# Performance work log

Measured on AMD Instinct MI355X. Metric: run time of the kernel, lower is better.

## Reference

```python
import jax, jax.numpy as jnp
import numpy as np

EPS = 1e-5

def binarize(w):
    # sign() binarization with straight-through estimator (identity grad)
    s = jnp.where(w >= 0, 1.0, -1.0).astype(w.dtype)
    return w + jax.lax.stop_gradient(s - w)

def batchnorm(x, gamma, beta):
    # BatchNorm1d in training mode: biased batch statistics over axis 0
    mean = jnp.mean(x, axis=0)
    var = jnp.mean(jnp.square(x - mean), axis=0)
    return (x - mean) * jax.lax.rsqrt(var + EPS) * gamma + beta

def setup_inputs() -> dict:
    key = jax.random.key(0)
    ks = jax.random.split(key, 3)
    B, D_IN, D_H, D_OUT = 65536, 784, 300, 10
    x = jax.random.normal(ks[0], (B, D_IN), dtype=jnp.float32)
    W1 = jax.random.normal(ks[1], (D_H, D_IN), dtype=jnp.float32) * 0.05
    W2 = jax.random.normal(ks[2], (D_OUT, D_H), dtype=jnp.float32) * 0.05
    gamma1 = jnp.ones((D_H,), jnp.float32)
    beta1 = jnp.zeros((D_H,), jnp.float32)
    gamma2 = jnp.ones((D_OUT,), jnp.float32)
    beta2 = jnp.zeros((D_OUT,), jnp.float32)
    return {"x": x, "W1": W1, "gamma1": gamma1, "beta1": beta1,
            "W2": W2, "gamma2": gamma2, "beta2": beta2}

def reference(x, W1, gamma1, beta1, W2, gamma2, beta2):
    h = x @ binarize(W1).T            # [B, 300]
    h = batchnorm(h, gamma1, beta1)
    o = h @ binarize(W2).T            # [B, 10]
    return batchnorm(o, gamma2, beta2)
```

## Files before the change

kernel.cpp:

```cpp
#include <hip/hip_runtime.h>
#include <cstdint>
#include <cstddef>

#define B_ROWS 65536
#define D_IN   784
#define KP     800
#define D_H    300
#define NP     320
#define D_OUT  10
#define NP2    16
#define EPS    1e-5f
#define NBLK   1024
#define APAD   44

typedef _Float16 half8  __attribute__((ext_vector_type(8)));
typedef float    floatx4 __attribute__((ext_vector_type(4)));

#define OFF_S1   ((size_t)0)
#define OFF_H    ((size_t)512000)
#define OFF_ST1  (OFF_H + (size_t)41943040)
#define OFF_W2   (OFF_ST1 + (size_t)2560)
#define OFF_ST2  (OFF_W2 + (size_t)10240)
#define OFF_OC   (OFF_ST2 + (size_t)256)
#define OFF_P1   OFF_OC
#define OFF_P2   (OFF_OC + (size_t)4194304)

__global__ void k_prep1(const float* __restrict__ W1, _Float16* __restrict__ S1)
{
    int idx = blockIdx.x * 256 + threadIdx.x;
    int n = idx / KP;
    int k = idx - n * KP;
    float v = 0.0f;
    if (n < D_H && k < D_IN)
        v = (W1[n * D_IN + k] >= 0.0f) ? 1.0f : -1.0f;
    S1[idx] = (_Float16)v;
}


#define PF_B(BV, NK)                                                        \
    _Pragma("unroll")                                                       \
    for (int nt = 0; nt < 5; ++nt)                                          \
        BV[nt] = *(const half8*)(bb + (size_t)nt * 16 * KP + (NK));

#define STAGE_LOAD(KK)                                                      \
    {                                                                       \
        sv0 = (floatx4){}; sv1 = (floatx4){};                               \
        if ((KK) + sc < D_IN) {               \
            sv0 = *(const floatx4*)(sxp + (KK));                            \
            sv1 = *(const floatx4*)(sxp + (KK) + 4);                        \
        }                                                                   \
    }

#define STAGE_STORE(BUF)                                                    \
    {                                                                       \
        half8 hv;                                                           \
        _Pragma("unroll")                                                   \
        for (int i2 = 0; i2 < 4; ++i2) {                                    \
            hv[i2]     = (_Float16)sv0[i2];                                 \
            hv[4 + i2] = (_Float16)sv1[i2];                                 \
        }                                                                   \
        *(half8*)&Alds[BUF][srow][sc] = hv;                                 \
    }

#define AFRAG(BUF)                                                          \
    _Pragma("unroll")                                                       \
    for (int mt = 0; mt < 4; ++mt)                                          \
        a[mt] = *(const half8*)&Alds[BUF][mt * 16 + row15][quad * 8];

#define COMPUTE(BV)                                                         \
    _Pragma("unroll")                                                       \
    for (int nt = 0; nt < 5; ++nt)                                          \
        _Pragma("unroll")                                                   \
        for (int mt = 0; mt < 4; ++mt)                                      \
            acc[mt][nt] = __builtin_amdgcn_mfma_f32_16x16x32_f16(           \
                a[mt], BV[nt], acc[mt][nt], 0, 0, 0);

__global__ __launch_bounds__(256) void k_gemm1(const float* __restrict__ x,
                                               const _Float16* __restrict__ S1,
                                               _Float16* __restrict__ h,
                                               float* __restrict__ part)
{
    __shared__ _Float16 Alds[2][64][APAD];
    const int t     = threadIdx.x;
    const int wave  = t >> 6;
    const int lane  = t & 63;
    const int row15 = lane & 15;
    const int quad  = lane >> 4;
    const int m0    = blockIdx.x * 64;

    const int srow = t >> 2;
    const int sc   = (t & 3) * 8;
    const float* sxp = x + (size_t)(m0 + srow) * D_IN + sc;

    const _Float16* bb = S1 + (size_t)(wave * 80 + row15) * KP + quad * 8;

    floatx4 acc[4][5] = {};
    half8   b0[5], b1[5];
    half8   a[4];
    floatx4 sv0, sv1;

    STAGE_LOAD(0)
    STAGE_STORE(0)
    PF_B(b0, 0)
    __syncthreads();

    for (int i = 0; i < 12; ++i) {
        const int kk = i * 64;
        STAGE_LOAD(kk + 32)
        PF_B(b1, kk + 32)
        AFRAG(0)
        COMPUTE(b0)
        STAGE_STORE(1)
        __syncthreads();
        STAGE_LOAD(kk + 64)
        PF_B(b0, kk + 64)
        AFRAG(1)
        COMPUTE(b1)
        STAGE_STORE(0)
        __syncthreads();
    }
    AFRAG(0)
    COMPUTE(b0)

    float s[5] = {}, q[5] = {};
#pragma unroll
    for (int mt = 0; mt < 4; ++mt)
#pragma unroll
        for (int nt = 0; nt < 5; ++nt)
#pragma unroll
            for (int r = 0; r < 4; ++r) {
                float v = acc[mt][nt][r];
                int m = m0 + mt * 16 + quad * 4 + r;
                int n = wave * 80 + nt * 16 + row15;
                h[(size_t)m * NP + n] = (_Float16)v;
                s[nt] += v;
                q[nt] += v * v;
            }
#pragma unroll
    for (int nt = 0; nt < 5; ++nt) {
        s[nt] += __shfl_xor(s[nt], 16); s[nt] += __shfl_xor(s[nt], 32);
        q[nt] += __shfl_xor(q[nt], 16); q[nt] += __shfl_xor(q[nt], 32);
    }
    if (quad == 0) {
#pragma unroll
        for (int nt = 0; nt < 5; ++nt) {
            int col = wave * 80 + nt * 16 + row15;
            part[(size_t)col * NBLK + blockIdx.x]        = s[nt];
            part[(size_t)(NP + col) * NBLK + blockIdx.x] = q[nt];
        }
    }
}

__global__ void k_reduce(const float* __restrict__ part, float* __restrict__ st)
{
    __shared__ float red[4];
    const int c = blockIdx.x;
    const int t = threadIdx.x;
    const float* p = part + (size_t)c * NBLK;
    float s = p[t] + p[t + 256] + p[t + 512] + p[t + 768];
#pragma unroll
    for (int off = 1; off < 64; off <<= 1) s += __shfl_xor(s, off);
    if ((t & 63) == 0) red[t >> 6] = s;
    __syncthreads();
    if (t == 0) st[c] = red[0] + red[1] + red[2] + red[3];
}

__global__ void k_prep2(const float* __restrict__ st, const float* __restrict__ gamma1,
                        const float* __restrict__ W2, _Float16* __restrict__ w2h)
{
    int j = threadIdx.x;
    float mean = st[j] * (1.0f / 65536.0f);
    float var  = st[NP + j] * (1.0f / 65536.0f) - mean * mean;
    float a1   = 0.0f;
    if (j < D_H) a1 = gamma1[j] / sqrtf(var + EPS);
    for (int k = 0; k < NP2; ++k) {
        float w = 0.0f;
        if (k < D_OUT && j < D_H)
            w = (W2[k * D_H + j] >= 0.0f) ? a1 : -a1;
        w2h[k * NP + j] = (_Float16)w;
    }
}

__global__ __launch_bounds__(256) void k_gemm2(const _Float16* __restrict__ h,
                                               const _Float16* __restrict__ w2h,
                                               float* __restrict__ oc,
                                               float* __restrict__ part2)
{
    __shared__ _Float16 Wlds[16][328];
    __shared__ float reds[4][16], redq[4][16];
    const int t     = threadIdx.x;
    const int wave  = t >> 6;
    const int lane  = t & 63;
    const int row15 = lane & 15;
    const int quad  = lane >> 4;

    for (int c = t; c < 640; c += 256) {
        int r  = c / 40;
        int cc = (c - r * 40) * 8;
        *(half8*)&Wlds[r][cc] = *(const half8*)(w2h + r * NP + cc);
    }
    __syncthreads();

    const int m0 = blockIdx.x * 64 + wave * 16;
    const _Float16* hp = h + (size_t)(m0 + row15) * NP + quad * 8;
    floatx4 acc = {};
#pragma unroll
    for (int kk = 0; kk < NP; kk += 32) {
        half8 a2 = *(const half8*)(hp + kk);
        half8 b2 = *(const half8*)&Wlds[row15][kk + quad * 8];
        acc = __builtin_amdgcn_mfma_f32_16x16x32_f16(a2, b2, acc, 0, 0, 0);
    }
    float s = 0.f, q = 0.f;
#pragma unroll
    for (int r = 0; r < 4; ++r) {
        float v = acc[r];
        oc[(size_t)(m0 + quad * 4 + r) * NP2 + row15] = v;
        s += v; q += v * v;
    }
    s += __shfl_xor(s, 16); s += __shfl_xor(s, 32);
    q += __shfl_xor(q, 16); q += __shfl_xor(q, 32);
    if (lane < 16) { reds[wave][row15] = s; redq[wave][row15] = q; }
    __syncthreads();
    if (t < 16) {
        float S = reds[0][t] + reds[1][t] + reds[2][t] + reds[3][t];
        float Q = redq[0][t] + redq[1][t] + redq[2][t] + redq[3][t];
        part2[(size_t)t * NBLK + blockIdx.x]          = S;
        part2[(size_t)(16 + t) * NBLK + blockIdx.x]   = Q;
    }
}

__global__ void k_final(const float* __restrict__ oc, const float* __restrict__ st2,
                        const float* __restrict__ gamma2, const float* __restrict__ beta2,
                        float* __restrict__ out)
{
    int idx = blockIdx.x * 256 + threadIdx.x;
    int m = idx / 10;
    int k = idx - m * 10;
    float mean = st2[k] * (1.0f / 65536.0f);
    float var  = st2[16 + k] * (1.0f / 65536.0f) - mean * mean;
    float sc   = gamma2[k] / sqrtf(var + EPS);
    out[idx] = (oc[(size_t)m * NP2 + k] - mean) * sc + beta2[k];
}

extern "C" void kernel_launch(void* const* d_in, const int* in_sizes, int n_in,
                              void* d_out, int out_size, void* d_ws, size_t ws_size,
                              hipStream_t stream)
{
    const float* x      = (const float*)d_in[0];
    const float* W1     = (const float*)d_in[1];
    const float* gamma1 = (const float*)d_in[2];
    const float* W2     = (const float*)d_in[4];
    const float* gamma2 = (const float*)d_in[5];
    const float* beta2  = (const float*)d_in[6];
    float* out = (float*)d_out;

    char* ws = (char*)d_ws;
    _Float16* S1    = (_Float16*)(ws + OFF_S1);
    _Float16* h     = (_Float16*)(ws + OFF_H);
    float*    st1   = (float*)(ws + OFF_ST1);
    _Float16* w2h   = (_Float16*)(ws + OFF_W2);
    float*    st2   = (float*)(ws + OFF_ST2);
    float*    oc    = (float*)(ws + OFF_OC);
    float*    part  = (float*)(ws + OFF_P1);
    float*    part2 = (float*)(ws + OFF_P2);

    k_prep1 <<<1000, 256, 0, stream>>>(W1, S1);
    k_gemm1 <<<NBLK, 256, 0, stream>>>(x, S1, h, part);
    k_reduce<<<640, 256, 0, stream>>>(part, st1);
    k_prep2 <<<1, 320, 0, stream>>>(st1, gamma1, W2, w2h);
    k_gemm2 <<<NBLK, 256, 0, stream>>>(h, w2h, oc, part2);
    k_reduce<<<32, 256, 0, stream>>>(part2, st2);
    k_final <<<2560, 256, 0, stream>>>(oc, st2, gamma2, beta2, out);
}
```

Measured before the change: 94.96 us.

## Load GEMM1 A fragments directly from global memory, dropping LDS staging

The first GEMM no longer stages x tiles through double-buffered shared memory with block-wide barriers. Each wave now loads its A fragments straight from global memory into registers and converts them to fp16 in place. This removes the LDS writes, the LDS reads and the __syncthreads calls. The cost is that all four waves of a block load the same 64 rows of x, so global/L2 traffic for x rises and more registers are used. The K tail past 784 is handled by re-reading valid columns at an in-bounds offset; those values are multiplied by zero-padded B entries, so they contribute nothing.

```diff
diff --git a/kernel.cpp b/kernel.cpp
--- a/kernel.cpp
+++ b/kernel.cpp
@@ -11,7 +11,6 @@
 #define NP2    16
 #define EPS    1e-5f
 #define NBLK   1024
-#define APAD   44
 
 typedef _Float16 half8  __attribute__((ext_vector_type(8)));
 typedef float    floatx4 __attribute__((ext_vector_type(4)));
@@ -42,30 +41,24 @@
     for (int nt = 0; nt < 5; ++nt)                                          \
         BV[nt] = *(const half8*)(bb + (size_t)nt * 16 * KP + (NK));
 
-#define STAGE_LOAD(KK)                                                      \
-    {                                                                       \
-        sv0 = (floatx4){}; sv1 = (floatx4){};                               \
-        if ((KK) + sc < D_IN) {               \
-            sv0 = *(const floatx4*)(sxp + (KK));                            \
-            sv1 = *(const floatx4*)(sxp + (KK) + 4);                        \
-        }                                                                   \
-    }
-
-#define STAGE_STORE(BUF)                                                    \
-    {                                                                       \
+#define ALOAD(AV, OFF)                                                      \
+    _Pragma("unroll")                                                       \
+    for (int mt = 0; mt < 4; ++mt) {                                        \
+        AV[2 * mt]     = *(const floatx4*)(axp[mt] + (OFF));                \
+        AV[2 * mt + 1] = *(const floatx4*)(axp[mt] + (OFF) + 4);            \
+    }
+
+#define ACVT(AV)                                                            \
+    _Pragma("unroll")                                                       \
+    for (int mt = 0; mt < 4; ++mt) {                                        \
         half8 hv;                                                           \
         _Pragma("unroll")                                                   \
         for (int i2 = 0; i2 < 4; ++i2) {                                    \
-            hv[i2]     = (_Float16)sv0[i2];                                 \
-            hv[4 + i2] = (_Float16)sv1[i2];                                 \
+            hv[i2]     = (_Float16)AV[2 * mt][i2];                          \
+            hv[4 + i2] = (_Float16)AV[2 * mt + 1][i2];                      \
         }                                                                   \
-        *(half8*)&Alds[BUF][srow][sc] = hv;                                 \
-    }
-
-#define AFRAG(BUF)                                                          \
-    _Pragma("unroll")                                                       \
-    for (int mt = 0; mt < 4; ++mt)                                          \
-        a[mt] = *(const half8*)&Alds[BUF][mt * 16 + row15][quad * 8];
+        a[mt] = hv;                                                         \
+    }
 
 #define COMPUTE(BV)                                                         \
     _Pragma("unroll")                                                       \
@@ -80,7 +73,6 @@
                                                _Float16* __restrict__ h,
                                                float* __restrict__ part)
 {
-    __shared__ _Float16 Alds[2][64][APAD];
     const int t     = threadIdx.x;
     const int wave  = t >> 6;
     const int lane  = t & 63;
@@ -88,38 +80,35 @@
     const int quad  = lane >> 4;
     const int m0    = blockIdx.x * 64;
 
-    const int srow = t >> 2;
-    const int sc   = (t & 3) * 8;
-    const float* sxp = x + (size_t)(m0 + srow) * D_IN + sc;
+    const float* axp[4];
+#pragma unroll
+    for (int mt = 0; mt < 4; ++mt)
+        axp[mt] = x + (size_t)(m0 + mt * 16 + row15) * D_IN + quad * 8;
+    const int tailoff = (quad < 2) ? 768 : -(quad * 8);
 
     const _Float16* bb = S1 + (size_t)(wave * 80 + row15) * KP + quad * 8;
 
     floatx4 acc[4][5] = {};
+    floatx4 av0[8], av1[8];
     half8   b0[5], b1[5];
     half8   a[4];
-    floatx4 sv0, sv1;
-
-    STAGE_LOAD(0)
-    STAGE_STORE(0)
+
+    ALOAD(av0, 0)
     PF_B(b0, 0)
-    __syncthreads();
 
     for (int i = 0; i < 12; ++i) {
         const int kk = i * 64;
-        STAGE_LOAD(kk + 32)
+        ALOAD(av1, kk + 32)
         PF_B(b1, kk + 32)
-        AFRAG(0)
+        ACVT(av0)
         COMPUTE(b0)
-        STAGE_STORE(1)
-        __syncthreads();
-        STAGE_LOAD(kk + 64)
+        const int off2 = (i == 11) ? tailoff : (kk + 64);
+        ALOAD(av0, off2)
         PF_B(b0, kk + 64)
-        AFRAG(1)
+        ACVT(av1)
         COMPUTE(b1)
-        STAGE_STORE(0)
-        __syncthreads();
-    }
-    AFRAG(0)
+    }
+    ACVT(av0)
     COMPUTE(b0)
 
     float s[5] = {}, q[5] = {};
```

After: 130.2 us. 37.1% more time.
